# Performance work log

Hardware: AMD Instinct MI355X
Metric: run time of the kernel (lower is better)

The kernel has to match this reference:

```python
import jax, jax.numpy as jnp
import numpy as np

B, S, D, H, L, F, V, P = 256, 64, 768, 12, 12, 3072, 32000, 768
HD = D // H  # head_dim = 64
EPS = 1e-6


def _ln(x, g, b):
    m = jnp.mean(x, axis=-1, keepdims=True)
    v = jnp.var(x, axis=-1, keepdims=True)
    return (x - m) * jax.lax.rsqrt(v + EPS) * g + b


def setup_inputs() -> dict:
    key = jax.random.key(0)
    ks = jax.random.split(key, 16)
    s = 0.02
    f = lambda k, shp: (jax.random.normal(k, shp) * s).astype(jnp.float32)
    return dict(
        input_ids=jax.random.randint(ks[0], (B, S), 0, V, dtype=jnp.int32),
        attention_mask=jnp.ones((B, S), dtype=jnp.int32),
        tok_emb=f(ks[1], (V, D)),
        pos_emb=f(ks[2], (S, D)),  # max_position_embeddings == S == 64
        ln1_g=jnp.ones((L, D)), ln1_b=jnp.zeros((L, D)),
        wq=f(ks[3], (L, D, D)), bq=jnp.zeros((L, D)),
        wk=f(ks[4], (L, D, D)), bk=jnp.zeros((L, D)),
        wv=f(ks[5], (L, D, D)), bv=jnp.zeros((L, D)),
        wo=f(ks[6], (L, D, D)), bo=jnp.zeros((L, D)),
        ln2_g=jnp.ones((L, D)), ln2_b=jnp.zeros((L, D)),
        w1=f(ks[7], (L, D, F)), b1=jnp.zeros((L, F)),
        w2=f(ks[8], (L, F, D)), b2=jnp.zeros((L, D)),
        fln_g=jnp.ones((D,)), fln_b=jnp.zeros((D,)),
        head_w=f(ks[9], (D, P)), head_b=jnp.zeros((P,)),
    )


def reference(input_ids, attention_mask, tok_emb, pos_emb, ln1_g, ln1_b,
              wq, bq, wk, bk, wv, bv, wo, bo, ln2_g, ln2_b,
              w1, b1, w2, b2, fln_g, fln_b, head_w, head_b):
    # Embeddings: token + learned position
    h = tok_emb[input_ids] + pos_emb[None, :, :]  # [B,S,D]
    # _prepare_4d_attention_mask: 0 where mask==1, dtype-min where mask==0
    neg = jnp.finfo(jnp.float32).min
    mask4d = jnp.where(attention_mask[:, None, None, :] == 0, neg, 0.0).astype(jnp.float32)  # [B,1,1,S]
    scale = HD ** -0.5

    def layer(h, p):
        l1g, l1b, Wq, Bq, Wk, Bk, Wv, Bv, Wo, Bo, l2g, l2b, W1, B1, W2, B2 = p
        x = _ln(h, l1g, l1b)
        q = (x @ Wq + Bq).reshape(B, S, H, HD)
        k = (x @ Wk + Bk).reshape(B, S, H, HD)
        v = (x @ Wv + Bv).reshape(B, S, H, HD)
        scores = jnp.einsum('bqhd,bkhd->bhqk', q, k) * scale + mask4d
        attn = jax.nn.softmax(scores.astype(jnp.float32), axis=-1).astype(h.dtype)
        o = jnp.einsum('bhqk,bkhd->bqhd', attn, v).reshape(B, S, D)
        h = h + (o @ Wo + Bo)
        x = _ln(h, l2g, l2b)
        h = h + (jax.nn.gelu(x @ W1 + B1, approximate=True) @ W2 + B2)
        return h, None

    h, _ = jax.lax.scan(layer, h, (ln1_g, ln1_b, wq, bq, wk, bk, wv, bv,
                                   wo, bo, ln2_g, ln2_b, w1, b1, w2, b2))
    last_hidden = _ln(h, fln_g, fln_b)
    pooled = last_hidden[:, -1, :] @ head_w + head_b  # EOS-pooled head
    return last_hidden, pooled
```

## Files before the change

kernel.cpp:

```cpp
#include <hip/hip_runtime.h>
#include <hip/hip_bf16.h>

typedef __attribute__((ext_vector_type(8))) short short8;
typedef __attribute__((ext_vector_type(4))) float f32x4;
typedef unsigned short u16;
typedef unsigned int u32;

#define L_ 12
#define D_ 768
#define F_ 3072
#define M_ 16384
#define P_ 768
#define NQKV 2304

__device__ __forceinline__ u16 f2bf(float f) {
  __hip_bfloat16 h = __float2bfloat16(f);
  return __builtin_bit_cast(u16, h);
}

__device__ __forceinline__ f32x4 mfma_bf16(short8 a, short8 b, f32x4 c) {
  return __builtin_amdgcn_mfma_f32_16x16x32_bf16(a, b, c, 0, 0, 0);
}

__device__ __forceinline__ float gelu_tanh(float x) {
  float u = 0.7978845608028654f * (x + 0.044715f * x * x * x);
  float e = __expf(2.0f * u);
  float t = 1.0f - 2.0f / (e + 1.0f);
  return 0.5f * x * (1.0f + t);
}

__device__ __forceinline__ void glds16(const void* g, void* l) {
  __builtin_amdgcn_global_load_lds(
      (const __attribute__((address_space(1))) u32*)g,
      (__attribute__((address_space(3))) u32*)l, 16, 0, 0);
}

__global__ __launch_bounds__(256) void wtrans_kernel(
    const float* __restrict__ src, u16* __restrict__ dst, int R, int C, size_t dzs)
{
  __shared__ float tile[32][33];
  const float* s = src + (size_t)blockIdx.z * R * C;
  u16* d = dst + (size_t)blockIdx.z * dzs;
  const int c0 = blockIdx.x * 32, r0 = blockIdx.y * 32;
  const int tx = threadIdx.x, ty = threadIdx.y;
#pragma unroll
  for (int i = 0; i < 32; i += 8)
    tile[ty + i][tx] = s[(size_t)(r0 + ty + i) * C + c0 + tx];
  __syncthreads();
#pragma unroll
  for (int i = 0; i < 32; i += 8)
    d[(size_t)(c0 + ty + i) * R + r0 + tx] = f2bf(tile[tx][ty + i]);
}

__global__ __launch_bounds__(256) void fusebias_kernel(
    const float* __restrict__ bq, const float* __restrict__ bk,
    const float* __restrict__ bv, float* __restrict__ out)
{
  const int i = blockIdx.x * 256 + threadIdx.x;
  if (i >= L_ * NQKV) return;
  const int l = i / NQKV, c = i - l * NQKV;
  float v;
  if (c < 768) v = bq[l * 768 + c];
  else if (c < 1536) v = bk[l * 768 + c - 768];
  else v = bv[l * 768 + c - 1536];
  out[i] = v;
}

__global__ __launch_bounds__(256) void embed_kernel(
    const int* __restrict__ ids, const float* __restrict__ tok,
    const float* __restrict__ pos, float* __restrict__ h)
{
  const int idx = blockIdx.x * 256 + threadIdx.x;
  const int t = idx / 192;
  const int c = (idx - t * 192) * 4;
  const int s = t & 63;
  const int id = ids[t];
  const float4 te = *(const float4*)(tok + (size_t)id * 768 + c);
  const float4 pe = *(const float4*)(pos + (size_t)s * 768 + c);
  float4 r; r.x = te.x + pe.x; r.y = te.y + pe.y; r.z = te.z + pe.z; r.w = te.w + pe.w;
  *(float4*)&h[(size_t)t * 768 + c] = r;
}

template<bool FOUT>
__global__ __launch_bounds__(256) void ln_kernel(
    const float* __restrict__ hin, const float* __restrict__ g,
    const float* __restrict__ bt, u16* __restrict__ xout, float* __restrict__ fout)
{
  const int row = blockIdx.x * 4 + (threadIdx.x >> 6);
  const int lane = threadIdx.x & 63;
  const float* hr = hin + (size_t)row * 768;
  const float4 va = *(const float4*)(hr + lane * 4);
  const float4 vb = *(const float4*)(hr + 256 + lane * 4);
  const float4 vc = *(const float4*)(hr + 512 + lane * 4);
  float s  = va.x + va.y + va.z + va.w + vb.x + vb.y + vb.z + vb.w + vc.x + vc.y + vc.z + vc.w;
  float s2 = va.x * va.x + va.y * va.y + va.z * va.z + va.w * va.w
           + vb.x * vb.x + vb.y * vb.y + vb.z * vb.z + vb.w * vb.w
           + vc.x * vc.x + vc.y * vc.y + vc.z * vc.z + vc.w * vc.w;
#pragma unroll
  for (int mk = 1; mk < 64; mk <<= 1) { s += __shfl_xor(s, mk, 64); s2 += __shfl_xor(s2, mk, 64); }
  const float mean = s * (1.f / 768.f);
  const float rstd = rsqrtf(s2 * (1.f / 768.f) - mean * mean + 1e-6f);
#pragma unroll
  for (int j = 0; j < 3; ++j) {
    const int c = j * 256 + lane * 4;
    const float4 x4 = (j == 0) ? va : ((j == 1) ? vb : vc);
    const float4 g4 = *(const float4*)(g + c);
    const float4 b4 = *(const float4*)(bt + c);
    const float o0 = (x4.x - mean) * rstd * g4.x + b4.x;
    const float o1 = (x4.y - mean) * rstd * g4.y + b4.y;
    const float o2 = (x4.z - mean) * rstd * g4.z + b4.z;
    const float o3 = (x4.w - mean) * rstd * g4.w + b4.w;
    ushort4 ub; ub.x = f2bf(o0); ub.y = f2bf(o1); ub.z = f2bf(o2); ub.w = f2bf(o3);
    *(ushort4*)&xout[(size_t)row * 768 + c] = ub;
    if (FOUT) {
      float4 f4; f4.x = o0; f4.y = o1; f4.z = o2; f4.w = o3;
      *(float4*)&fout[(size_t)row * 768 + c] = f4;
    }
  }
}

template<int EPI>
__global__ __launch_bounds__(256) void gemm_kernel(
    const u16* __restrict__ A, int lda, const u16* __restrict__ BT,
    const float* __restrict__ bias, const float* __restrict__ resid,
    void* __restrict__ outp, int M, int N, int K)
{
  __shared__ __align__(16) u16 sA[2][4096];
  __shared__ __align__(16) u16 sB[2][4096];
  const int tid = threadIdx.x, lane = tid & 63, wid = tid >> 6;
  const int wr = wid >> 1, wc = wid & 1;
  const int l15 = lane & 15, l4 = lane >> 4;

  const int nbx = gridDim.x;
  const int nwg = nbx * gridDim.y;
  const int orig = blockIdx.x + nbx * blockIdx.y;
  const int q8 = nwg >> 3, r8 = nwg & 7;
  const int xcd = orig & 7, idx = orig >> 3;
  const int wgid = (xcd < r8 ? xcd * (q8 + 1) : r8 * (q8 + 1) + (xcd - r8) * q8) + idx;
  const int m0 = (wgid / nbx) * 128;
  const int n0 = (wgid - (wgid / nbx) * nbx) * 128;

  f32x4 acc[4][4];
#pragma unroll
  for (int i = 0; i < 4; ++i)
#pragma unroll
    for (int j = 0; j < 4; ++j) acc[i][j] = (f32x4){0.f, 0.f, 0.f, 0.f};

  const char* gA0 = (const char*)(A + (size_t)(m0 + (tid >> 2)) * lda + (tid & 3) * 8);
  const char* gA1 = (const char*)(A + (size_t)(m0 + 64 + (tid >> 2)) * lda + (tid & 3) * 8);
  const char* gB0 = (const char*)(BT + (size_t)(n0 + (tid >> 2)) * K + (tid & 3) * 8);
  const char* gB1 = (const char*)(BT + (size_t)(n0 + 64 + (tid >> 2)) * K + (tid & 3) * 8);
  const int lofs = wid * 512;

  auto stage = [&](int buf) {
    glds16(gA0, sA[buf] + lofs); glds16(gA1, sA[buf] + 2048 + lofs);
    glds16(gB0, sB[buf] + lofs); glds16(gB1, sB[buf] + 2048 + lofs);
    gA0 += 64; gA1 += 64; gB0 += 64; gB1 += 64;
  };

  const int arow = wr * 64 + l15, brow = wc * 64 + l15, koff = l4 * 8;
  const int niter = K >> 5;

  stage(0);
  __syncthreads();

#pragma unroll 2
  for (int t = 0; t < niter - 1; ++t) {
    const int cur = t & 1;
    stage(cur ^ 1);
    short8 af[4], bfv[4];
#pragma unroll
    for (int i = 0; i < 4; ++i) af[i] = *(const short8*)&sA[cur][(arow + i * 16) * 32 + koff];
#pragma unroll
    for (int j = 0; j < 4; ++j) bfv[j] = *(const short8*)&sB[cur][(brow + j * 16) * 32 + koff];
#pragma unroll
    for (int i = 0; i < 4; ++i)
#pragma unroll
      for (int j = 0; j < 4; ++j)
        acc[i][j] = mfma_bf16(af[i], bfv[j], acc[i][j]);
    __syncthreads();
  }
  {
    const int cur = (niter - 1) & 1;
    short8 af[4], bfv[4];
#pragma unroll
    for (int i = 0; i < 4; ++i) af[i] = *(const short8*)&sA[cur][(arow + i * 16) * 32 + koff];
#pragma unroll
    for (int j = 0; j < 4; ++j) bfv[j] = *(const short8*)&sB[cur][(brow + j * 16) * 32 + koff];
#pragma unroll
    for (int i = 0; i < 4; ++i)
#pragma unroll
      for (int j = 0; j < 4; ++j)
        acc[i][j] = mfma_bf16(af[i], bfv[j], acc[i][j]);
  }

  const int r0 = m0 + wr * 64 + l4 * 4;
  const int c0 = n0 + wc * 64 + l15;
#pragma unroll
  for (int i = 0; i < 4; ++i) {
#pragma unroll
    for (int j = 0; j < 4; ++j) {
      const int col = c0 + j * 16;
      const float bv = bias[col];
#pragma unroll
      for (int e = 0; e < 4; ++e) {
        const int row = r0 + i * 16 + e;
        float val = acc[i][j][e] + bv;
        if constexpr (EPI == 0) {
          ((u16*)outp)[(size_t)row * N + col] = f2bf(val);
        } else if constexpr (EPI == 1) {
          ((float*)outp)[(size_t)row * N + col] = val + resid[(size_t)row * N + col];
        } else if constexpr (EPI == 2) {
          ((u16*)outp)[(size_t)row * N + col] = f2bf(gelu_tanh(val));
        } else {
          ((float*)outp)[(size_t)row * N + col] = val;
        }
      }
    }
  }
}

__global__ __launch_bounds__(256) void attn_kernel(
    const u16* __restrict__ qkv, const int* __restrict__ amask, u16* __restrict__ o)
{
  __shared__ __align__(16) u16 sQ[64 * 80];
  __shared__ __align__(16) u16 sK[64 * 80];
  __shared__ __align__(16) u16 sVT[64 * 80];
  __shared__ __align__(16) u16 sP[4][16 * 80];

  const int bh = blockIdx.x;
  const int b = bh / 12;
  const int h = bh - b * 12;
  const int tid = threadIdx.x, lane = tid & 63, wid = tid >> 6;
  const int l15 = lane & 15, l4 = lane >> 4;
  const size_t base = (size_t)b * (64 * NQKV) + h * 64;
  const size_t obase = (size_t)b * (64 * 768) + h * 64;

  for (int c = tid; c < 512; c += 256) {
    const int row = c >> 3, d0 = (c & 7) * 8;
    *(uint4*)&sQ[row * 80 + d0] = *(const uint4*)(qkv + base + (size_t)row * NQKV + d0);
    *(uint4*)&sK[row * 80 + d0] = *(const uint4*)(qkv + base + 768 + (size_t)row * NQKV + d0);
  }
  for (int c = tid; c < 512; c += 256) {
    const int key = c & 63, d0 = (c >> 6) * 8;
    const uint4 t4 = *(const uint4*)(qkv + base + 1536 + (size_t)key * NQKV + d0);
    const u16* pe = (const u16*)&t4;
#pragma unroll
    for (int e = 0; e < 8; ++e) sVT[(d0 + e) * 80 + key] = pe[e];
  }
  __syncthreads();

  const int qrow = wid * 16 + l15;
  const short8 qa0 = *(const short8*)&sQ[qrow * 80 + l4 * 8];
  const short8 qa1 = *(const short8*)&sQ[qrow * 80 + 32 + l4 * 8];
  f32x4 sc[4];
#pragma unroll
  for (int jf = 0; jf < 4; ++jf) {
    sc[jf] = (f32x4){0.f, 0.f, 0.f, 0.f};
    const short8 kb0 = *(const short8*)&sK[(jf * 16 + l15) * 80 + l4 * 8];
    const short8 kb1 = *(const short8*)&sK[(jf * 16 + l15) * 80 + 32 + l4 * 8];
    sc[jf] = mfma_bf16(qa0, kb0, sc[jf]);
    sc[jf] = mfma_bf16(qa1, kb1, sc[jf]);
  }
  float mv[4];
#pragma unroll
  for (int jf = 0; jf < 4; ++jf)
    mv[jf] = (amask[b * 64 + jf * 16 + l15] == 0) ? -3.402823466e38f : 0.f;

  float rsum[4];
#pragma unroll
  for (int e = 0; e < 4; ++e) {
    const float s0 = sc[0][e] * 0.125f + mv[0];
    const float s1 = sc[1][e] * 0.125f + mv[1];
    const float s2 = sc[2][e] * 0.125f + mv[2];
    const float s3 = sc[3][e] * 0.125f + mv[3];
    float mx = fmaxf(fmaxf(s0, s1), fmaxf(s2, s3));
#pragma unroll
    for (int mk = 1; mk < 16; mk <<= 1) mx = fmaxf(mx, __shfl_xor(mx, mk, 64));
    const float p0 = __expf(s0 - mx), p1 = __expf(s1 - mx);
    const float p2 = __expf(s2 - mx), p3 = __expf(s3 - mx);
    float sm = p0 + p1 + p2 + p3;
#pragma unroll
    for (int mk = 1; mk < 16; mk <<= 1) sm += __shfl_xor(sm, mk, 64);
    rsum[e] = sm;
    const int prow = l4 * 4 + e;
    sP[wid][prow * 80 +  0 + l15] = f2bf(p0);
    sP[wid][prow * 80 + 16 + l15] = f2bf(p1);
    sP[wid][prow * 80 + 32 + l15] = f2bf(p2);
    sP[wid][prow * 80 + 48 + l15] = f2bf(p3);
  }
  __syncthreads();

  const short8 pa0 = *(const short8*)&sP[wid][l15 * 80 + l4 * 8];
  const short8 pa1 = *(const short8*)&sP[wid][l15 * 80 + 32 + l4 * 8];
#pragma unroll
  for (int jf = 0; jf < 4; ++jf) {
    f32x4 oc = (f32x4){0.f, 0.f, 0.f, 0.f};
    const short8 vb0 = *(const short8*)&sVT[(jf * 16 + l15) * 80 + l4 * 8];
    const short8 vb1 = *(const short8*)&sVT[(jf * 16 + l15) * 80 + 32 + l4 * 8];
    oc = mfma_bf16(pa0, vb0, oc);
    oc = mfma_bf16(pa1, vb1, oc);
#pragma unroll
    for (int e = 0; e < 4; ++e) {
      const int row = wid * 16 + l4 * 4 + e;
      o[obase + (size_t)row * 768 + jf * 16 + l15] = f2bf(oc[e] / rsum[e]);
    }
  }
}

extern "C" void kernel_launch(void* const* d_in, const int* in_sizes, int n_in,
                              void* d_out, int out_size, void* d_ws, size_t ws_size,
                              hipStream_t stream)
{
  (void)in_sizes; (void)n_in; (void)out_size; (void)ws_size;
  const int*   ids  = (const int*)  d_in[0];
  const int*   am   = (const int*)  d_in[1];
  const float* tok  = (const float*)d_in[2];
  const float* pos  = (const float*)d_in[3];
  const float* ln1g = (const float*)d_in[4];
  const float* ln1b = (const float*)d_in[5];
  const float* wq   = (const float*)d_in[6];
  const float* bq   = (const float*)d_in[7];
  const float* wk   = (const float*)d_in[8];
  const float* bk   = (const float*)d_in[9];
  const float* wv   = (const float*)d_in[10];
  const float* bv   = (const float*)d_in[11];
  const float* wo   = (const float*)d_in[12];
  const float* bo   = (const float*)d_in[13];
  const float* ln2g = (const float*)d_in[14];
  const float* ln2b = (const float*)d_in[15];
  const float* w1   = (const float*)d_in[16];
  const float* b1   = (const float*)d_in[17];
  const float* w2   = (const float*)d_in[18];
  const float* b2   = (const float*)d_in[19];
  const float* flng = (const float*)d_in[20];
  const float* flnb = (const float*)d_in[21];
  const float* hw   = (const float*)d_in[22];
  const float* hb   = (const float*)d_in[23];

  char* ws = (char*)d_ws;
  size_t off = 0;
  auto alloc = [&](size_t bytes) -> char* {
    char* p = ws + off; off += (bytes + 255) & ~(size_t)255; return p;
  };
  u16* wqkvT = (u16*)alloc((size_t)L_ * NQKV * D_ * 2);
  u16* woT = (u16*)alloc((size_t)L_ * D_ * D_ * 2);
  u16* w1T = (u16*)alloc((size_t)L_ * D_ * F_ * 2);
  u16* w2T = (u16*)alloc((size_t)L_ * D_ * F_ * 2);
  u16* hwT = (u16*)alloc((size_t)D_ * P_ * 2);
  float* bqkv = (float*)alloc((size_t)L_ * NQKV * 4);
  float* h = (float*)alloc((size_t)M_ * D_ * 4);
  u16* xb   = (u16*)alloc((size_t)M_ * D_ * 2);
  u16* qkvb = (u16*)alloc((size_t)M_ * NQKV * 2);
  u16* ob   = (u16*)alloc((size_t)M_ * D_ * 2);
  u16* m1   = (u16*)alloc((size_t)M_ * F_ * 2);

  const dim3 tb32(32, 8);
  const size_t LQKV = (size_t)NQKV * D_;
  wtrans_kernel<<<dim3(24, 24, 12), tb32, 0, stream>>>(wq, wqkvT,            768, 768, LQKV);
  wtrans_kernel<<<dim3(24, 24, 12), tb32, 0, stream>>>(wk, wqkvT + 589824,   768, 768, LQKV);
  wtrans_kernel<<<dim3(24, 24, 12), tb32, 0, stream>>>(wv, wqkvT + 1179648,  768, 768, LQKV);
  wtrans_kernel<<<dim3(24, 24, 12), tb32, 0, stream>>>(wo, woT, 768, 768, (size_t)D_ * D_);
  wtrans_kernel<<<dim3(96, 24, 12), tb32, 0, stream>>>(w1, w1T, 768, 3072, (size_t)D_ * F_);
  wtrans_kernel<<<dim3(24, 96, 12), tb32, 0, stream>>>(w2, w2T, 3072, 768, (size_t)D_ * F_);
  wtrans_kernel<<<dim3(24, 24, 1),  tb32, 0, stream>>>(hw, hwT, 768, 768, (size_t)D_ * P_);
  fusebias_kernel<<<108, 256, 0, stream>>>(bq, bk, bv, bqkv);

  embed_kernel<<<12288, 256, 0, stream>>>(ids, tok, pos, h);

  for (int l = 0; l < 12; ++l) {
    ln_kernel<false><<<4096, 256, 0, stream>>>(h, ln1g + l * 768, ln1b + l * 768, xb, nullptr);
    gemm_kernel<0><<<dim3(18, 128), 256, 0, stream>>>(xb, 768, wqkvT + (size_t)l * LQKV,
                                                      bqkv + l * NQKV, nullptr, qkvb, M_, NQKV, 768);
    attn_kernel<<<3072, 256, 0, stream>>>(qkvb, am, ob);
    gemm_kernel<1><<<dim3(6, 128), 256, 0, stream>>>(ob, 768, woT + (size_t)l * 589824, bo + l * 768, h, h, M_, 768, 768);
    ln_kernel<false><<<4096, 256, 0, stream>>>(h, ln2g + l * 768, ln2b + l * 768, xb, nullptr);
    gemm_kernel<2><<<dim3(24, 128), 256, 0, stream>>>(xb, 768, w1T + (size_t)l * 2359296, b1 + l * 3072, nullptr, m1, M_, 3072, 768);
    gemm_kernel<1><<<dim3(6, 128), 256, 0, stream>>>(m1, 3072, w2T + (size_t)l * 2359296, b2 + l * 768, h, h, M_, 768, 3072);
  }

  ln_kernel<true><<<4096, 256, 0, stream>>>(h, flng, flnb, xb, (float*)d_out);
  gemm_kernel<3><<<dim3(6, 2), 256, 0, stream>>>(xb + 63 * 768, 64 * 768, hwT, hb, nullptr,
                                                 (float*)d_out + (size_t)M_ * D_, 256, 768, 768);
}
```

Baseline: 5.418 ms.

## Add 256x256-tile GEMM kernel with swizzled LDS and staged MFMA schedule

Adds a new GEMM kernel using 256x256 output tiles, 512 threads, BK=64 double-buffered LDS (128KB) with XOR swizzle, and a quadrant-wise MFMA schedule with explicit barriers, waitcnts and setprio. All four per-layer GEMMs (QKV, out-proj, FFN up and down) switch to it. Larger tiles raise arithmetic intensity and cut global traffic per FLOP, and the swizzle is meant to avoid LDS bank conflicts. The cost is that 128KB of LDS allows only one block per CU despite launch_bounds(512,2), and grids shrink (e.g. 192 blocks for the N=768 GEMMs), which risks underfilling a 256-CU device.

After: 5.063 ms. 6.5% less time.

```diff
diff --git a/kernel.cpp b/kernel.cpp
--- a/kernel.cpp
+++ b/kernel.cpp
@@ -34,6 +34,10 @@
       (const __attribute__((address_space(1))) u32*)g,
       (__attribute__((address_space(3))) u32*)l, 16, 0, 0);
 }
+
+#define LGKM0 do { asm volatile("s_waitcnt lgkmcnt(0)" ::: "memory"); \
+                   __builtin_amdgcn_sched_barrier(0); } while (0)
+#define VM0   asm volatile("s_waitcnt vmcnt(0)" ::: "memory")
 
 __global__ __launch_bounds__(256) void wtrans_kernel(
     const float* __restrict__ src, u16* __restrict__ dst, int R, int C, size_t dzs)
@@ -120,6 +124,145 @@
 }
 
 template<int EPI>
+__global__ __launch_bounds__(512, 2) void gemm256_kernel(
+    const u16* __restrict__ A, int lda, const u16* __restrict__ BT,
+    const float* __restrict__ bias, const float* __restrict__ resid,
+    void* __restrict__ outp, int M, int N, int K)
+{
+  __shared__ __align__(16) char lds[131072];
+  const int tid = threadIdx.x, lane = tid & 63, wid = tid >> 6;
+  const int wm = wid >> 2, wn = wid & 3;
+  const int l15 = lane & 15, l4 = lane >> 4;
+
+  const int nbx = gridDim.x, nwg = nbx * gridDim.y;
+  const int orig = blockIdx.x + nbx * blockIdx.y;
+  const int q8 = nwg >> 3, r8 = nwg & 7;
+  const int xcd = orig & 7, cidx = orig >> 3;
+  const int wg = (xcd < r8 ? xcd * (q8 + 1) : r8 * (q8 + 1) + (xcd - r8) * q8) + cidx;
+  const int m0 = (wg / nbx) * 256;
+  const int n0 = (wg - (wg / nbx) * nbx) * 256;
+
+  f32x4 acc[8][4];
+#pragma unroll
+  for (int i = 0; i < 8; ++i)
+#pragma unroll
+    for (int j = 0; j < 4; ++j) acc[i][j] = (f32x4){0.f, 0.f, 0.f, 0.f};
+
+  const int g1 = tid + 512;
+  const int r0s = tid >> 3, r1s = g1 >> 3;
+  const int c0s = (tid & 7) ^ (r0s & 7), c1s = (g1 & 7) ^ (r1s & 7);
+  const int aoff0 = r0s * lda + c0s * 8, aoff1 = r1s * lda + c1s * 8;
+  const int boff0 = r0s * K + c0s * 8, boff1 = r1s * K + c1s * 8;
+  const u16* Abase = A + (size_t)m0 * lda;
+  const u16* Bbase = BT + (size_t)n0 * K;
+  const int ldsw = wid * 1024;
+
+  auto stageTile = [&](int b, int kt) {
+    const u16* Ak = Abase + kt;
+    const u16* Bk = Bbase + kt;
+    char* LA = lds + b * 65536;
+    char* LB = LA + 32768;
+    glds16(Ak + aoff0, LA + ldsw);
+    glds16(Ak + aoff1, LA + 8192 + ldsw);
+    glds16(Ak + 128 * lda + aoff0, LA + 16384 + ldsw);
+    glds16(Ak + 128 * lda + aoff1, LA + 16384 + 8192 + ldsw);
+    glds16(Bk + boff0, LB + ldsw);
+    glds16(Bk + boff1, LB + 8192 + ldsw);
+    glds16(Bk + 128 * K + boff0, LB + 16384 + ldsw);
+    glds16(Bk + 128 * K + boff1, LB + 16384 + 8192 + ldsw);
+  };
+
+  const int sw = l15 & 7;
+  const int cs0 = (l4 ^ sw) << 4;
+  const int cs1 = ((4 + l4) ^ sw) << 4;
+  const int aRdRow = wm * 16384 + l15 * 128;
+  const int bRdRow = 32768 + (wn >> 1) * 16384 + ((wn & 1) * 64 + l15) * 128;
+
+  short8 af[4][2], bn0[2][2], bn1[2][2];
+
+  auto loadA = [&](const char* Lb, int mq) {
+#pragma unroll
+    for (int mf = 0; mf < 4; ++mf) {
+      af[mf][0] = *(const short8*)(Lb + aRdRow + mq * 8192 + mf * 2048 + cs0);
+      af[mf][1] = *(const short8*)(Lb + aRdRow + mq * 8192 + mf * 2048 + cs1);
+    }
+  };
+  auto loadB = [&](const char* Lb, int nq, short8 (&bf)[2][2]) {
+#pragma unroll
+    for (int nf = 0; nf < 2; ++nf) {
+      bf[nf][0] = *(const short8*)(Lb + bRdRow + nq * 4096 + nf * 2048 + cs0);
+      bf[nf][1] = *(const short8*)(Lb + bRdRow + nq * 4096 + nf * 2048 + cs1);
+    }
+  };
+  auto mmaQ = [&](int mq, int nq, short8 (&bf)[2][2]) {
+#pragma unroll
+    for (int mf = 0; mf < 4; ++mf)
+#pragma unroll
+      for (int nf = 0; nf < 2; ++nf)
+#pragma unroll
+        for (int ks = 0; ks < 2; ++ks)
+          acc[mq * 4 + mf][nq * 2 + nf] =
+              mfma_bf16(af[mf][ks], bf[nf][ks], acc[mq * 4 + mf][nq * 2 + nf]);
+  };
+
+  const int nt = K >> 6;
+
+  auto ktile = [&](int b, int t) {
+    const char* Lb = lds + b * 65536;
+    if (t + 1 < nt) stageTile(b ^ 1, (t + 1) << 6);
+    loadA(Lb, 0);
+    loadB(Lb, 0, bn0);
+    __builtin_amdgcn_s_barrier();
+    LGKM0;
+    __builtin_amdgcn_s_setprio(1); mmaQ(0, 0, bn0); __builtin_amdgcn_s_setprio(0);
+    __builtin_amdgcn_s_barrier();
+    loadB(Lb, 1, bn1);
+    __builtin_amdgcn_s_barrier();
+    LGKM0;
+    __builtin_amdgcn_s_setprio(1); mmaQ(0, 1, bn1); __builtin_amdgcn_s_setprio(0);
+    __builtin_amdgcn_s_barrier();
+    loadA(Lb, 1);
+    __builtin_amdgcn_s_barrier();
+    LGKM0;
+    __builtin_amdgcn_s_setprio(1); mmaQ(1, 1, bn1); __builtin_amdgcn_s_setprio(0);
+    __builtin_amdgcn_s_barrier();
+    __builtin_amdgcn_s_setprio(1); mmaQ(1, 0, bn0); __builtin_amdgcn_s_setprio(0);
+    VM0;
+    __builtin_amdgcn_s_barrier();
+  };
+
+  stageTile(0, 0);
+  VM0;
+  __builtin_amdgcn_s_barrier();
+  for (int t = 0; t < nt; t += 2) { ktile(0, t); ktile(1, t + 1); }
+
+  const int rbase = m0 + wm * 128 + l4 * 4;
+  const int cbase = n0 + wn * 64 + l15;
+#pragma unroll
+  for (int mi = 0; mi < 8; ++mi) {
+#pragma unroll
+    for (int ni = 0; ni < 4; ++ni) {
+      const int col = cbase + (ni >> 1) * 32 + (ni & 1) * 16;
+      const float bv = bias[col];
+#pragma unroll
+      for (int e = 0; e < 4; ++e) {
+        const int row = rbase + (mi >> 2) * 64 + (mi & 3) * 16 + e;
+        float val = acc[mi][ni][e] + bv;
+        if constexpr (EPI == 0) {
+          ((u16*)outp)[(size_t)row * N + col] = f2bf(val);
+        } else if constexpr (EPI == 1) {
+          ((float*)outp)[(size_t)row * N + col] = val + resid[(size_t)row * N + col];
+        } else if constexpr (EPI == 2) {
+          ((u16*)outp)[(size_t)row * N + col] = f2bf(gelu_tanh(val));
+        } else {
+          ((float*)outp)[(size_t)row * N + col] = val;
+        }
+      }
+    }
+  }
+}
+
+template<int EPI>
 __global__ __launch_bounds__(256) void gemm_kernel(
     const u16* __restrict__ A, int lda, const u16* __restrict__ BT,
     const float* __restrict__ bias, const float* __restrict__ resid,
@@ -168,30 +311,30 @@
   for (int t = 0; t < niter - 1; ++t) {
     const int cur = t & 1;
     stage(cur ^ 1);
-    short8 af[4], bfv[4];
-#pragma unroll
-    for (int i = 0; i < 4; ++i) af[i] = *(const short8*)&sA[cur][(arow + i * 16) * 32 + koff];
+    short8 afv[4], bfv[4];
+#pragma unroll
+    for (int i = 0; i < 4; ++i) afv[i] = *(const short8*)&sA[cur][(arow + i * 16) * 32 + koff];
 #pragma unroll
     for (int j = 0; j < 4; ++j) bfv[j] = *(const short8*)&sB[cur][(brow + j * 16) * 32 + koff];
 #pragma unroll
     for (int i = 0; i < 4; ++i)
 #pragma unroll
       for (int j = 0; j < 4; ++j)
-        acc[i][j] = mfma_bf16(af[i], bfv[j], acc[i][j]);
+        acc[i][j] = mfma_bf16(afv[i], bfv[j], acc[i][j]);
     __syncthreads();
   }
   {
     const int cur = (niter - 1) & 1;
-    short8 af[4], bfv[4];
-#pragma unroll
-    for (int i = 0; i < 4; ++i) af[i] = *(const short8*)&sA[cur][(arow + i * 16) * 32 + koff];
+    short8 afv[4], bfv[4];
+#pragma unroll
+    for (int i = 0; i < 4; ++i) afv[i] = *(const short8*)&sA[cur][(arow + i * 16) * 32 + koff];
 #pragma unroll
     for (int j = 0; j < 4; ++j) bfv[j] = *(const short8*)&sB[cur][(brow + j * 16) * 32 + koff];
 #pragma unroll
     for (int i = 0; i < 4; ++i)
 #pragma unroll
       for (int j = 0; j < 4; ++j)
-        acc[i][j] = mfma_bf16(af[i], bfv[j], acc[i][j]);
+        acc[i][j] = mfma_bf16(afv[i], bfv[j], acc[i][j]);
   }
 
   const int r0 = m0 + wr * 64 + l4 * 4;
@@ -370,13 +513,16 @@
 
   for (int l = 0; l < 12; ++l) {
     ln_kernel<false><<<4096, 256, 0, stream>>>(h, ln1g + l * 768, ln1b + l * 768, xb, nullptr);
-    gemm_kernel<0><<<dim3(18, 128), 256, 0, stream>>>(xb, 768, wqkvT + (size_t)l * LQKV,
-                                                      bqkv + l * NQKV, nullptr, qkvb, M_, NQKV, 768);
+    gemm256_kernel<0><<<dim3(9, 64), 512, 0, stream>>>(xb, 768, wqkvT + (size_t)l * LQKV,
+                                                       bqkv + l * NQKV, nullptr, qkvb, M_, NQKV, 768);
     attn_kernel<<<3072, 256, 0, stream>>>(qkvb, am, ob);
-    gemm_kernel<1><<<dim3(6, 128), 256, 0, stream>>>(ob, 768, woT + (size_t)l * 589824, bo + l * 768, h, h, M_, 768, 768);
+    gemm256_kernel<1><<<dim3(3, 64), 512, 0, stream>>>(ob, 768, woT + (size_t)l * 589824,
+                                                       bo + l * 768, h, h, M_, 768, 768);
     ln_kernel<false><<<4096, 256, 0, stream>>>(h, ln2g + l * 768, ln2b + l * 768, xb, nullptr);
-    gemm_kernel<2><<<dim3(24, 128), 256, 0, stream>>>(xb, 768, w1T + (size_t)l * 2359296, b1 + l * 3072, nullptr, m1, M_, 3072, 768);
-    gemm_kernel<1><<<dim3(6, 128), 256, 0, stream>>>(m1, 3072, w2T + (size_t)l * 2359296, b2 + l * 768, h, h, M_, 768, 3072);
+    gemm256_kernel<2><<<dim3(12, 64), 512, 0, stream>>>(xb, 768, w1T + (size_t)l * 2359296,
+                                                        b1 + l * 3072, nullptr, m1, M_, 3072, 768);
+    gemm256_kernel<1><<<dim3(3, 64), 512, 0, stream>>>(m1, 3072, w2T + (size_t)l * 2359296,
+                                                       b2 + l * 768, h, h, M_, 768, 3072);
   }
 
   ln_kernel<true><<<4096, 256, 0, stream>>>(h, flng, flnb, xb, (float*)d_out);
```
